# Kernel optimization log

Hardware: AMD Instinct MI355X
Metric: run time of the kernel (lower is better)

Reference implementation:

```python
import jax, jax.numpy as jnp
import numpy as np

DIM = 2048
DIM_HEAD = 128
HEADS = 16
FF_MULT = 4
ATTN_INNER = DIM_HEAD * HEADS            # 2048
FF_INNER = DIM * FF_MULT                 # 8192
FUSED_OUT = ATTN_INNER + 2 * DIM_HEAD + 2 * FF_INNER  # 18688
EPS = 1e-5


def setup_inputs() -> dict:
    key = jax.random.key(0)
    ks = jax.random.split(key, 5)
    B, N = 1, 2048
    x = jax.random.normal(ks[0], (B, N, DIM), dtype=jnp.float32)
    gamma = jnp.ones((DIM,), dtype=jnp.float32)
    # store weights as [in, out] for x @ W
    w_fused = jax.random.normal(ks[1], (DIM, FUSED_OUT), dtype=jnp.float32) * (DIM ** -0.5)
    w_attn_out = jax.random.normal(ks[2], (ATTN_INNER, DIM), dtype=jnp.float32) * (ATTN_INNER ** -0.5)
    w_ff_out = jax.random.normal(ks[3], (FF_INNER, DIM), dtype=jnp.float32) * (FF_INNER ** -0.5)
    return {"x": x, "gamma": gamma, "w_fused": w_fused,
            "w_attn_out": w_attn_out, "w_ff_out": w_ff_out}


def reference(x, gamma, w_fused, w_attn_out, w_ff_out):
    b, n, d = x.shape
    h, dh = HEADS, DIM_HEAD
    scale = dh ** -0.5

    # LayerNorm (beta fixed at 0)
    mu = jnp.mean(x, axis=-1, keepdims=True)
    var = jnp.mean(jnp.square(x - mu), axis=-1, keepdims=True)
    xn = (x - mu) * jax.lax.rsqrt(var + EPS) * gamma

    # fused QKV + FF projection
    proj = xn @ w_fused  # [b, n, FUSED_OUT]
    q = proj[..., :ATTN_INNER]
    k = proj[..., ATTN_INNER:ATTN_INNER + dh]
    v = proj[..., ATTN_INNER + dh:ATTN_INNER + 2 * dh]
    ff = proj[..., ATTN_INNER + 2 * dh:]

    # multi-query attention: q per-head, k/v shared
    q = q.reshape(b, n, h, dh).transpose(0, 2, 1, 3) * scale  # [b,h,n,dh]
    sim = jnp.einsum('bhid,bjd->bhij', q, k)
    causal = jnp.triu(jnp.ones((n, n), dtype=bool), k=1)
    neg = -jnp.finfo(sim.dtype).max
    sim = jnp.where(causal, neg, sim)
    attn = jax.nn.softmax(sim, axis=-1)
    out = jnp.einsum('bhij,bjd->bhid', attn, v)
    out = out.transpose(0, 2, 1, 3).reshape(b, n, h * dh)
    attn_out = out @ w_attn_out

    # parallel SwiGLU FFN
    ff_x, gate = jnp.split(ff, 2, axis=-1)
    ff_out = (jax.nn.silu(gate) * ff_x) @ w_ff_out

    return attn_out + ff_out
```

## Files before the change

kernel.cpp:

```cpp
#include <hip/hip_runtime.h>
#include <hip/hip_bf16.h>

typedef unsigned short u16;
typedef __bf16 bf16x8 __attribute__((ext_vector_type(8)));
typedef float f32x4 __attribute__((ext_vector_type(4)));

#define DIM 2048
#define SEQ 2048
#define HEADS 16
#define DH 128
#define FUSED_OUT 18688
#define FF_INNER 8192
#define KOFF 2048
#define VOFF 2176
#define FFOFF 2304
#define AE_LD 10240

#define WS_XN   0
#define WS_WFT  8388608
#define WS_PROJ 84934656
#define WS_VT   161480704
#define WS_BTE  0
#define WS_AE   41943040

__device__ __forceinline__ float b2f(u16 u) {
  union { unsigned int i; float f; } c; c.i = ((unsigned int)u) << 16; return c.f;
}
__device__ __forceinline__ u16 f2b(float f) {
  union { float f; unsigned int i; } c; c.f = f;
  return (u16)((c.i + 0x7fffu + ((c.i >> 16) & 1u)) >> 16);
}
__device__ __forceinline__ void async16(void* lds, const void* g) {
  __builtin_amdgcn_global_load_lds((const __attribute__((address_space(1))) unsigned int*)g,
                                   (__attribute__((address_space(3))) unsigned int*)lds,
                                   16, 0, 0);
}

union U8 { uint4 v; u16 s[8]; };

__global__ void __launch_bounds__(256) ln_kernel(const float* __restrict__ x,
                                                 const float* __restrict__ gamma,
                                                 u16* __restrict__ xn) {
  const int row = blockIdx.x, tid = threadIdx.x;
  const int lane = tid & 63, wv = tid >> 6;
  float v[8], s1 = 0.f, s2 = 0.f;
  {
    float4 a0 = *(const float4*)(x + (size_t)row * DIM + tid * 8);
    float4 a1 = *(const float4*)(x + (size_t)row * DIM + tid * 8 + 4);
    v[0] = a0.x; v[1] = a0.y; v[2] = a0.z; v[3] = a0.w;
    v[4] = a1.x; v[5] = a1.y; v[6] = a1.z; v[7] = a1.w;
  }
#pragma unroll
  for (int i = 0; i < 8; ++i) { s1 += v[i]; s2 += v[i] * v[i]; }
#pragma unroll
  for (int off = 32; off > 0; off >>= 1) {
    s1 += __shfl_down(s1, off, 64);
    s2 += __shfl_down(s2, off, 64);
  }
  __shared__ float r1[4], r2[4];
  if (lane == 0) { r1[wv] = s1; r2[wv] = s2; }
  __syncthreads();
  s1 = r1[0] + r1[1] + r1[2] + r1[3];
  s2 = r2[0] + r2[1] + r2[2] + r2[3];
  const float inv = 1.0f / DIM;
  const float mu = s1 * inv;
  const float var = s2 * inv - mu * mu;
  const float rs = rsqrtf(var + 1e-5f);
  float4 g0 = *(const float4*)(gamma + tid * 8);
  float4 g1 = *(const float4*)(gamma + tid * 8 + 4);
  const float gm[8] = {g0.x, g0.y, g0.z, g0.w, g1.x, g1.y, g1.z, g1.w};
  U8 o;
#pragma unroll
  for (int i = 0; i < 8; ++i) o.s[i] = f2b((v[i] - mu) * rs * gm[i]);
  *(uint4*)(xn + (size_t)row * DIM + tid * 8) = o.v;
}

__global__ void __launch_bounds__(256) transpose_f2b(const float* __restrict__ in,
                                                     u16* __restrict__ out,
                                                     int ldin, int ldout) {
  __shared__ u16 t[32][33];
  const int tx = threadIdx.x, ty = threadIdx.y;
  const int r0 = blockIdx.y * 32, c0 = blockIdx.x * 32;
#pragma unroll
  for (int i = 0; i < 4; ++i)
    t[ty + i * 8][tx] = f2b(in[(size_t)(r0 + ty + i * 8) * ldin + c0 + tx]);
  __syncthreads();
#pragma unroll
  for (int i = 0; i < 4; ++i)
    out[(size_t)(c0 + ty + i * 8) * ldout + r0 + tx] = t[tx][ty + i * 8];
}

__global__ void __launch_bounds__(256) transpose_u16(const u16* __restrict__ in,
                                                     u16* __restrict__ out,
                                                     int ldin, int ldout) {
  __shared__ u16 t[32][33];
  const int tx = threadIdx.x, ty = threadIdx.y;
  const int r0 = blockIdx.y * 32, c0 = blockIdx.x * 32;
#pragma unroll
  for (int i = 0; i < 4; ++i)
    t[ty + i * 8][tx] = in[(size_t)(r0 + ty + i * 8) * ldin + c0 + tx];
  __syncthreads();
#pragma unroll
  for (int i = 0; i < 4; ++i)
    out[(size_t)(c0 + ty + i * 8) * ldout + r0 + tx] = t[tx][ty + i * 8];
}

template <bool OUTF32>
__global__ void __launch_bounds__(256) gemm_bt(const u16* __restrict__ A,
                                               const u16* __restrict__ Bt,
                                               void* __restrict__ Cv,
                                               int K, int lda, int ldb, int ldc) {
  __shared__ alignas(16) u16 sA[128 * 64];
  __shared__ alignas(16) u16 sB[128 * 64];
  const int tid = threadIdx.x;
  const int lane = tid & 63, wv = tid >> 6;
  const int lhalf = lane & 15, lgrp = lane >> 4;
  const int m0 = blockIdx.x * 128, n0 = blockIdx.y * 128;
  const int wr = (wv >> 1) * 64, wc = (wv & 1) * 64;
  const f32x4 fzero = {0.f, 0.f, 0.f, 0.f};

  const int srow = lane >> 3;
  const int scol = ((lane & 7) ^ srow) * 8;
  const int key = lhalf & 7;

  f32x4 acc[4][4];
#pragma unroll
  for (int i = 0; i < 4; ++i)
#pragma unroll
    for (int j = 0; j < 4; ++j) acc[i][j] = fzero;

  for (int k0 = 0; k0 < K; k0 += 64) {
#pragma unroll
    for (int c = 0; c < 4; ++c) {
      const int row = c * 32 + wv * 8 + srow;
      const int ldsoff = (c * 4096 + wv * 1024) >> 1;
      async16(&sA[ldsoff], A + (size_t)(m0 + row) * lda + k0 + scol);
      async16(&sB[ldsoff], Bt + (size_t)(n0 + row) * ldb + k0 + scol);
    }
    __syncthreads();
#pragma unroll
    for (int kk = 0; kk < 64; kk += 32) {
      bf16x8 af[4], bfr[4];
#pragma unroll
      for (int i = 0; i < 4; ++i)
        af[i] = *(const bf16x8*)&sA[(wr + i * 16 + lhalf) * 64 + ((((kk >> 3) + lgrp) ^ key) << 3)];
#pragma unroll
      for (int j = 0; j < 4; ++j)
        bfr[j] = *(const bf16x8*)&sB[(wc + j * 16 + lhalf) * 64 + ((((kk >> 3) + lgrp) ^ key) << 3)];
#pragma unroll
      for (int i = 0; i < 4; ++i)
#pragma unroll
        for (int j = 0; j < 4; ++j)
          acc[i][j] = __builtin_amdgcn_mfma_f32_16x16x32_bf16(af[i], bfr[j], acc[i][j], 0, 0, 0);
    }
    __syncthreads();
  }
#pragma unroll
  for (int i = 0; i < 4; ++i)
#pragma unroll
    for (int j = 0; j < 4; ++j)
#pragma unroll
      for (int t = 0; t < 4; ++t) {
        const int row = m0 + wr + i * 16 + lgrp * 4 + t;
        const int col = n0 + wc + j * 16 + lhalf;
        if (OUTF32) ((float*)Cv)[(size_t)row * ldc + col] = acc[i][j][t];
        else ((u16*)Cv)[(size_t)row * ldc + col] = f2b(acc[i][j][t]);
      }
}

__global__ void __launch_bounds__(256) attn_kernel(const u16* __restrict__ proj,
                                                   const u16* __restrict__ Vt,
                                                   u16* __restrict__ Ae) {
  const int h = blockIdx.y, qi = blockIdx.x;
  const int tid = threadIdx.x;
  const int lane = tid & 63, wv = tid >> 6;
  const int lhalf = lane & 15, lgrp = lane >> 4;
  const int key = lhalf & 7;

  __shared__ alignas(16) u16 Ks[128 * 128];
  __shared__ alignas(16) u16 Vts[128 * 128];
  __shared__ alignas(16) u16 Ps[4][16 * 128];

  bf16x8 aq[4];
  {
    const u16* gq = proj + (size_t)(qi * 64 + wv * 16 + lhalf) * FUSED_OUT + h * DH;
#pragma unroll
    for (int kk = 0; kk < 4; ++kk) aq[kk] = *(const bf16x8*)(gq + kk * 32 + lgrp * 8);
  }
  const f32x4 fzero = {0.f, 0.f, 0.f, 0.f};
  f32x4 o[8];
#pragma unroll
  for (int i = 0; i < 8; ++i) o[i] = fzero;
  float mrow[4] = {-__builtin_inff(), -__builtin_inff(), -__builtin_inff(), -__builtin_inff()};
  float lrow[4] = {0.f, 0.f, 0.f, 0.f};
  const float scale = 0.088388347648318447f;
  const int jmax = (qi * 64 + 63) >> 7;

  for (int jt = 0; jt <= jmax; ++jt) {
    __syncthreads();
#pragma unroll
    for (int i = 0; i < 8; ++i) {
      const int blk = i * 256 + tid;
      const int r = blk >> 4;
      const int b = blk & 15;
      const int c = (b ^ (r & 7)) * 8;
      *(uint4*)&Ks[r * 128 + c] = *(const uint4*)(proj + (size_t)(jt * 128 + r) * FUSED_OUT + KOFF + b * 8);
      *(uint4*)&Vts[r * 128 + c] = *(const uint4*)(Vt + (size_t)r * SEQ + jt * 128 + b * 8);
    }
    __syncthreads();
    f32x4 s[8];
#pragma unroll
    for (int sub = 0; sub < 8; ++sub) {
      f32x4 a = fzero;
#pragma unroll
      for (int kk = 0; kk < 4; ++kk) {
        bf16x8 bk = *(const bf16x8*)&Ks[(sub * 16 + lhalf) * 128 + (((kk * 4 + lgrp) ^ key) << 3)];
        a = __builtin_amdgcn_mfma_f32_16x16x32_bf16(aq[kk], bk, a, 0, 0, 0);
      }
      s[sub] = a;
    }
    const int row_g = qi * 64 + wv * 16 + lgrp * 4;
    const int col_b = jt * 128 + lhalf;
#pragma unroll
    for (int t = 0; t < 4; ++t) {
      float mx = -__builtin_inff();
#pragma unroll
      for (int sub = 0; sub < 8; ++sub) {
        float v = s[sub][t] * scale;
        if (col_b + sub * 16 > row_g + t) v = -__builtin_inff();
        s[sub][t] = v;
        mx = fmaxf(mx, v);
      }
      mx = fmaxf(mx, __shfl_xor(mx, 1, 64));
      mx = fmaxf(mx, __shfl_xor(mx, 2, 64));
      mx = fmaxf(mx, __shfl_xor(mx, 4, 64));
      mx = fmaxf(mx, __shfl_xor(mx, 8, 64));
      const float mnew = fmaxf(mrow[t], mx);
      const float alpha = __expf(mrow[t] - mnew);
      mrow[t] = mnew;
      float ls = 0.f;
#pragma unroll
      for (int sub = 0; sub < 8; ++sub) {
        const float p = __expf(s[sub][t] - mnew);
        s[sub][t] = p;
        ls += p;
      }
      ls += __shfl_xor(ls, 1, 64);
      ls += __shfl_xor(ls, 2, 64);
      ls += __shfl_xor(ls, 4, 64);
      ls += __shfl_xor(ls, 8, 64);
      lrow[t] = lrow[t] * alpha + ls;
      const int prow = lgrp * 4 + t;
      const int pkey = prow & 7;
#pragma unroll
      for (int sub = 0; sub < 8; ++sub) {
        o[sub][t] *= alpha;
        const int b = sub * 2 + (lhalf >> 3);
        Ps[wv][prow * 128 + ((b ^ pkey) << 3) + (lhalf & 7)] = f2b(s[sub][t]);
      }
    }
    __syncthreads();
#pragma unroll
    for (int kk = 0; kk < 4; ++kk) {
      bf16x8 ap = *(const bf16x8*)&Ps[wv][lhalf * 128 + (((kk * 4 + lgrp) ^ key) << 3)];
#pragma unroll
      for (int sub = 0; sub < 8; ++sub) {
        bf16x8 bv = *(const bf16x8*)&Vts[(sub * 16 + lhalf) * 128 + (((kk * 4 + lgrp) ^ key) << 3)];
        o[sub] = __builtin_amdgcn_mfma_f32_16x16x32_bf16(ap, bv, o[sub], 0, 0, 0);
      }
    }
  }
#pragma unroll
  for (int sub = 0; sub < 8; ++sub)
#pragma unroll
    for (int t = 0; t < 4; ++t) {
      const int row = qi * 64 + wv * 16 + lgrp * 4 + t;
      const int col = h * DH + sub * 16 + lhalf;
      Ae[(size_t)row * AE_LD + col] = f2b(o[sub][t] / lrow[t]);
    }
}

__global__ void __launch_bounds__(256) ffa_kernel(const u16* __restrict__ proj,
                                                  u16* __restrict__ Ae) {
  const size_t idx = (size_t)blockIdx.x * 256 + threadIdx.x;
  const size_t e = idx * 8;
  const int row = (int)(e >> 13);
  const int j = (int)(e & 8191);
  const u16* base = proj + (size_t)row * FUSED_OUT + FFOFF;
  U8 xr, gr, os;
  xr.v = *(const uint4*)(base + j);
  gr.v = *(const uint4*)(base + FF_INNER + j);
#pragma unroll
  for (int i = 0; i < 8; ++i) {
    const float g = b2f(gr.s[i]);
    const float sg = g / (1.f + __expf(-g));
    os.s[i] = f2b(sg * b2f(xr.s[i]));
  }
  *(uint4*)(Ae + (size_t)row * AE_LD + 2048 + j) = os.v;
}

extern "C" void kernel_launch(void* const* d_in, const int* in_sizes, int n_in,
                              void* d_out, int out_size, void* d_ws, size_t ws_size,
                              hipStream_t stream) {
  const float* x       = (const float*)d_in[0];
  const float* gamma   = (const float*)d_in[1];
  const float* w_fused = (const float*)d_in[2];
  const float* w_attn  = (const float*)d_in[3];
  const float* w_ff    = (const float*)d_in[4];
  float* out = (float*)d_out;
  char* ws = (char*)d_ws;
  u16* xn   = (u16*)(ws + WS_XN);
  u16* wfT  = (u16*)(ws + WS_WFT);
  u16* proj = (u16*)(ws + WS_PROJ);
  u16* Vt   = (u16*)(ws + WS_VT);
  u16* BtE  = (u16*)(ws + WS_BTE);
  u16* Ae   = (u16*)(ws + WS_AE);

  ln_kernel<<<dim3(2048), dim3(256), 0, stream>>>(x, gamma, xn);
  transpose_f2b<<<dim3(584, 64), dim3(32, 8), 0, stream>>>(w_fused, wfT, FUSED_OUT, DIM);
  gemm_bt<false><<<dim3(16, 146), dim3(256), 0, stream>>>(xn, wfT, proj, DIM, DIM, DIM, FUSED_OUT);

  transpose_u16<<<dim3(4, 64), dim3(32, 8), 0, stream>>>(proj + VOFF, Vt, FUSED_OUT, SEQ);
  transpose_f2b<<<dim3(64, 64), dim3(32, 8), 0, stream>>>(w_attn, BtE, DIM, AE_LD);
  transpose_f2b<<<dim3(64, 256), dim3(32, 8), 0, stream>>>(w_ff, BtE + 2048, DIM, AE_LD);
  attn_kernel<<<dim3(32, 16), dim3(256), 0, stream>>>(proj, Vt, Ae);
  ffa_kernel<<<dim3(8192), dim3(256), 0, stream>>>(proj, Ae);

  gemm_bt<true><<<dim3(16, 16), dim3(256), 0, stream>>>(Ae, BtE, out, AE_LD, AE_LD, AE_LD, DIM);
}
```

Measured before the change: 821.7 us.

## Split-K final GEMM, widen transposes, async attention loads, relax P barrier

The output projection GEMM is split along K into two halves that accumulate into a zeroed output with float atomics, doubling the block count. Weight and V transposes move to 64x64 tiles, and the two output-weight transposes merge into one launch. Attention K/V tile loads switch to async global-to-LDS copies, and the block barrier before the PV product becomes a wave-local LDS wait because each wave uses only its own P buffer. These changes trade extra atomic traffic and a memset for more parallelism and fewer launches.

```diff
diff --git a/kernel.cpp b/kernel.cpp
--- a/kernel.cpp
+++ b/kernel.cpp
@@ -75,47 +75,66 @@
   *(uint4*)(xn + (size_t)row * DIM + tid * 8) = o.v;
 }
 
-__global__ void __launch_bounds__(256) transpose_f2b(const float* __restrict__ in,
-                                                     u16* __restrict__ out,
-                                                     int ldin, int ldout) {
-  __shared__ u16 t[32][33];
+__global__ void __launch_bounds__(256) transpose_f2b64(const float* __restrict__ in,
+                                                       u16* __restrict__ out,
+                                                       int ldin, int ldout) {
+  __shared__ u16 t[64][65];
   const int tx = threadIdx.x, ty = threadIdx.y;
-  const int r0 = blockIdx.y * 32, c0 = blockIdx.x * 32;
-#pragma unroll
-  for (int i = 0; i < 4; ++i)
-    t[ty + i * 8][tx] = f2b(in[(size_t)(r0 + ty + i * 8) * ldin + c0 + tx]);
+  const int r0 = blockIdx.y * 64, c0 = blockIdx.x * 64;
+#pragma unroll
+  for (int i = 0; i < 16; ++i)
+    t[ty + i * 4][tx] = f2b(in[(size_t)(r0 + ty + i * 4) * ldin + c0 + tx]);
   __syncthreads();
 #pragma unroll
-  for (int i = 0; i < 4; ++i)
-    out[(size_t)(c0 + ty + i * 8) * ldout + r0 + tx] = t[tx][ty + i * 8];
-}
-
-__global__ void __launch_bounds__(256) transpose_u16(const u16* __restrict__ in,
-                                                     u16* __restrict__ out,
-                                                     int ldin, int ldout) {
-  __shared__ u16 t[32][33];
+  for (int i = 0; i < 16; ++i)
+    out[(size_t)(c0 + ty + i * 4) * ldout + r0 + tx] = t[tx][ty + i * 4];
+}
+
+__global__ void __launch_bounds__(256) trans_wout64(const float* __restrict__ w_attn,
+                                                    const float* __restrict__ w_ff,
+                                                    u16* __restrict__ BtE) {
+  __shared__ u16 t[64][65];
   const int tx = threadIdx.x, ty = threadIdx.y;
-  const int r0 = blockIdx.y * 32, c0 = blockIdx.x * 32;
-#pragma unroll
-  for (int i = 0; i < 4; ++i)
-    t[ty + i * 8][tx] = in[(size_t)(r0 + ty + i * 8) * ldin + c0 + tx];
+  const int c0 = blockIdx.x * 64;
+  const float* in; int r0, kout;
+  if (blockIdx.y < 32) { in = w_attn; r0 = blockIdx.y * 64; kout = r0; }
+  else { in = w_ff; r0 = (blockIdx.y - 32) * 64; kout = 2048 + r0; }
+#pragma unroll
+  for (int i = 0; i < 16; ++i)
+    t[ty + i * 4][tx] = f2b(in[(size_t)(r0 + ty + i * 4) * DIM + c0 + tx]);
   __syncthreads();
 #pragma unroll
-  for (int i = 0; i < 4; ++i)
-    out[(size_t)(c0 + ty + i * 8) * ldout + r0 + tx] = t[tx][ty + i * 8];
-}
-
-template <bool OUTF32>
+  for (int i = 0; i < 16; ++i)
+    BtE[(size_t)(c0 + ty + i * 4) * AE_LD + kout + tx] = t[tx][ty + i * 4];
+}
+
+__global__ void __launch_bounds__(256) transpose_u16_64(const u16* __restrict__ in,
+                                                        u16* __restrict__ out,
+                                                        int ldin, int ldout) {
+  __shared__ u16 t[64][65];
+  const int tx = threadIdx.x, ty = threadIdx.y;
+  const int r0 = blockIdx.y * 64, c0 = blockIdx.x * 64;
+#pragma unroll
+  for (int i = 0; i < 16; ++i)
+    t[ty + i * 4][tx] = in[(size_t)(r0 + ty + i * 4) * ldin + c0 + tx];
+  __syncthreads();
+#pragma unroll
+  for (int i = 0; i < 16; ++i)
+    out[(size_t)(c0 + ty + i * 4) * ldout + r0 + tx] = t[tx][ty + i * 4];
+}
+
+template <int OUTMODE>
 __global__ void __launch_bounds__(256) gemm_bt(const u16* __restrict__ A,
                                                const u16* __restrict__ Bt,
                                                void* __restrict__ Cv,
-                                               int K, int lda, int ldb, int ldc) {
+                                               int Ksz, int lda, int ldb, int ldc) {
   __shared__ alignas(16) u16 sA[128 * 64];
   __shared__ alignas(16) u16 sB[128 * 64];
   const int tid = threadIdx.x;
   const int lane = tid & 63, wv = tid >> 6;
   const int lhalf = lane & 15, lgrp = lane >> 4;
   const int m0 = blockIdx.x * 128, n0 = blockIdx.y * 128;
+  const int kbeg = blockIdx.z * Ksz, kend = kbeg + Ksz;
   const int wr = (wv >> 1) * 64, wc = (wv & 1) * 64;
   const f32x4 fzero = {0.f, 0.f, 0.f, 0.f};
 
@@ -129,7 +148,7 @@
 #pragma unroll
     for (int j = 0; j < 4; ++j) acc[i][j] = fzero;
 
-  for (int k0 = 0; k0 < K; k0 += 64) {
+  for (int k0 = kbeg; k0 < kend; k0 += 64) {
 #pragma unroll
     for (int c = 0; c < 4; ++c) {
       const int row = c * 32 + wv * 8 + srow;
@@ -163,8 +182,8 @@
       for (int t = 0; t < 4; ++t) {
         const int row = m0 + wr + i * 16 + lgrp * 4 + t;
         const int col = n0 + wc + j * 16 + lhalf;
-        if (OUTF32) ((float*)Cv)[(size_t)row * ldc + col] = acc[i][j][t];
-        else ((u16*)Cv)[(size_t)row * ldc + col] = f2b(acc[i][j][t]);
+        if (OUTMODE == 0) ((u16*)Cv)[(size_t)row * ldc + col] = f2b(acc[i][j][t]);
+        else atomicAdd((float*)Cv + (size_t)row * ldc + col, acc[i][j][t]);
       }
 }
 
@@ -181,6 +200,9 @@
   __shared__ alignas(16) u16 Vts[128 * 128];
   __shared__ alignas(16) u16 Ps[4][16 * 128];
 
+  const int sr = lane >> 4;
+  const int sb = lane & 15;
+
   bf16x8 aq[4];
   {
     const u16* gq = proj + (size_t)(qi * 64 + wv * 16 + lhalf) * FUSED_OUT + h * DH;
@@ -200,12 +222,11 @@
     __syncthreads();
 #pragma unroll
     for (int i = 0; i < 8; ++i) {
-      const int blk = i * 256 + tid;
-      const int r = blk >> 4;
-      const int b = blk & 15;
-      const int c = (b ^ (r & 7)) * 8;
-      *(uint4*)&Ks[r * 128 + c] = *(const uint4*)(proj + (size_t)(jt * 128 + r) * FUSED_OUT + KOFF + b * 8);
-      *(uint4*)&Vts[r * 128 + c] = *(const uint4*)(Vt + (size_t)r * SEQ + jt * 128 + b * 8);
+      const int ch = wv * 8 + i;
+      const int row = ch * 4 + sr;
+      const int gb = sb ^ (row & 7);
+      async16(&Ks[ch * 512], proj + (size_t)(jt * 128 + row) * FUSED_OUT + KOFF + gb * 8);
+      async16(&Vts[ch * 512], Vt + (size_t)row * SEQ + jt * 128 + gb * 8);
     }
     __syncthreads();
     f32x4 s[8];
@@ -259,7 +280,7 @@
         Ps[wv][prow * 128 + ((b ^ pkey) << 3) + (lhalf & 7)] = f2b(s[sub][t]);
       }
     }
-    __syncthreads();
+    asm volatile("s_waitcnt lgkmcnt(0)" ::: "memory");
 #pragma unroll
     for (int kk = 0; kk < 4; ++kk) {
       bf16x8 ap = *(const bf16x8*)&Ps[wv][lhalf * 128 + (((kk * 4 + lgrp) ^ key) << 3)];
@@ -316,15 +337,16 @@
   u16* BtE  = (u16*)(ws + WS_BTE);
   u16* Ae   = (u16*)(ws + WS_AE);
 
+  hipMemsetAsync(d_out, 0, (size_t)out_size * sizeof(float), stream);
+
   ln_kernel<<<dim3(2048), dim3(256), 0, stream>>>(x, gamma, xn);
-  transpose_f2b<<<dim3(584, 64), dim3(32, 8), 0, stream>>>(w_fused, wfT, FUSED_OUT, DIM);
-  gemm_bt<false><<<dim3(16, 146), dim3(256), 0, stream>>>(xn, wfT, proj, DIM, DIM, DIM, FUSED_OUT);
-
-  transpose_u16<<<dim3(4, 64), dim3(32, 8), 0, stream>>>(proj + VOFF, Vt, FUSED_OUT, SEQ);
-  transpose_f2b<<<dim3(64, 64), dim3(32, 8), 0, stream>>>(w_attn, BtE, DIM, AE_LD);
-  transpose_f2b<<<dim3(64, 256), dim3(32, 8), 0, stream>>>(w_ff, BtE + 2048, DIM, AE_LD);
+  transpose_f2b64<<<dim3(292, 32), dim3(64, 4), 0, stream>>>(w_fused, wfT, FUSED_OUT, DIM);
+  gemm_bt<0><<<dim3(16, 146, 1), dim3(256), 0, stream>>>(xn, wfT, proj, DIM, DIM, DIM, FUSED_OUT);
+
+  transpose_u16_64<<<dim3(2, 32), dim3(64, 4), 0, stream>>>(proj + VOFF, Vt, FUSED_OUT, SEQ);
+  trans_wout64<<<dim3(32, 160), dim3(64, 4), 0, stream>>>(w_attn, w_ff, BtE);
   attn_kernel<<<dim3(32, 16), dim3(256), 0, stream>>>(proj, Vt, Ae);
   ffa_kernel<<<dim3(8192), dim3(256), 0, stream>>>(proj, Ae);
 
-  gemm_bt<true><<<dim3(16, 16), dim3(256), 0, stream>>>(Ae, BtE, out, AE_LD, AE_LD, AE_LD, DIM);
-}
+  gemm_bt<2><<<dim3(16, 16, 2), dim3(256), 0, stream>>>(Ae, BtE, out, AE_LD / 2, AE_LD, AE_LD, DIM);
+}
```

Measured after the change: 718.4 us. 1.14x faster.
